# Kernel tuning notes

Measured on AMD Instinct MI355X. Metric: run time of the kernel, lower is better.

Reference implementation:

```python
import jax, jax.numpy as jnp
import numpy as np

T, B, D, H = 512, 64, 512, 512  # seq_len, batch, input_size, hidden_size


def setup_inputs() -> dict:
    key = jax.random.key(0)
    ks = jax.random.split(key, 7)
    s = jnp.float32(0.05)  # keep gates out of saturation
    return {
        "x": jax.random.normal(ks[0], (T, B, D), jnp.float32),
        "Wi_l0": jax.random.normal(ks[1], (2, 4 * H, D), jnp.float32) * s,
        "Wh_l0": jax.random.normal(ks[2], (2, 4 * H, H), jnp.float32) * s,
        "b_l0": jax.random.normal(ks[3], (2, 4 * H), jnp.float32) * s,
        "Wi_l1": jax.random.normal(ks[4], (2, 4 * H, 2 * H), jnp.float32) * s,
        "Wh_l1": jax.random.normal(ks[5], (2, 4 * H, H), jnp.float32) * s,
        "b_l1": jax.random.normal(ks[6], (2, 4 * H), jnp.float32) * s,
    }


def _lstm_dir(xs, Wi, Wh, b):
    """Run one LSTM direction over xs: [T, B, Din] -> ([T, B, H], h_T, c_T)."""
    Bsz = xs.shape[1]
    Hh = Wh.shape[-1]
    # Precompute input contribution for all timesteps (the big GEMM).
    gx = jnp.einsum('tbd,gd->tbg', xs, Wi) + b  # [T, B, 4H]

    def step(carry, gx_t):
        h, c = carry
        gates = gx_t + h @ Wh.T  # [B, 4H]
        i, f, g, o = jnp.split(gates, 4, axis=-1)
        c = jax.nn.sigmoid(f) * c + jax.nn.sigmoid(i) * jnp.tanh(g)
        h = jax.nn.sigmoid(o) * jnp.tanh(c)
        return (h, c), h

    h0 = jnp.zeros((Bsz, Hh), xs.dtype)
    (hT, cT), hs = jax.lax.scan(step, (h0, h0), gx)
    return hs, hT, cT


def _bilstm_layer(xs, Wi, Wh, b):
    hf, hTf, cTf = _lstm_dir(xs, Wi[0], Wh[0], b[0])
    hb, hTb, cTb = _lstm_dir(xs[::-1], Wi[1], Wh[1], b[1])
    # torch.stack(dim=2).view(T, B, -1) == concat along feature axis
    out = jnp.concatenate([hf, hb[::-1]], axis=-1)  # [T, B, 2H]
    return out, (hTf, hTb), (cTf, cTb)


def reference(x, Wi_l0, Wh_l0, b_l0, Wi_l1, Wh_l1, b_l1):
    o0, h0s, c0s = _bilstm_layer(x, Wi_l0, Wh_l0, b_l0)
    o1, h1s, c1s = _bilstm_layer(o0, Wi_l1, Wh_l1, b_l1)
    # state order: (layer0 fwd, layer0 bwd, layer1 fwd, layer1 bwd)
    h_n = jnp.stack(h0s + h1s, axis=0)  # [4, B, H]
    c_n = jnp.stack(c0s + c1s, axis=0)  # [4, B, H]
    return o1, (h_n, c_n)
```

## Files before the change

kernel.cpp:

```cpp
#include <hip/hip_runtime.h>
#include <stdint.h>


#define TT 512
#define BATCH 64
#define HH 512
#define NWG 64
#define NCOLS 32

typedef __attribute__((ext_vector_type(8))) short vshort8;
typedef __attribute__((ext_vector_type(4))) float vfloat4;

__device__ __forceinline__ vfloat4 mfma16(vshort8 a, vshort8 b, vfloat4 c) {
    return __builtin_amdgcn_mfma_f32_16x16x32_bf16(a, b, c, 0, 0, 0);
}

__device__ __forceinline__ float sigmoidf_(float x) {
    return 1.f / (1.f + __expf(-x));
}
__device__ __forceinline__ float tanhf_(float x) {
    float e = __expf(2.f * x);
    return 1.f - 2.f / (e + 1.f);
}
__device__ __forceinline__ unsigned short f2bf(float f) {
    uint32_t u = __float_as_uint(f);
    uint32_t r = (u + 0x7fffu + ((u >> 16) & 1u)) >> 16;
    return (unsigned short)r;
}

__global__ void cvt_f32_bf16(const float* __restrict__ src,
                             unsigned short* __restrict__ dst, int n) {
    int i = (blockIdx.x * blockDim.x + threadIdx.x) * 4;
    if (i + 3 < n) {
        float4 v = *(const float4*)(src + i);
        uint2 p;
        p.x = (uint32_t)f2bf(v.x) | ((uint32_t)f2bf(v.y) << 16);
        p.y = (uint32_t)f2bf(v.z) | ((uint32_t)f2bf(v.w) << 16);
        *(uint2*)(dst + i) = p;
    }
}

template <int DIN, bool WRITE_BF16>
__launch_bounds__(256, 1)
__global__ void lstm_phase(const unsigned short* __restrict__ A,
                           const unsigned short* __restrict__ Wi,
                           const float* __restrict__ Whf,
                           const float* __restrict__ bias,
                           unsigned short* __restrict__ hbuf,
                           uint32_t* __restrict__ cnt,
                           unsigned short* __restrict__ obf,
                           float* __restrict__ of32,
                           float* __restrict__ hn,
                           float* __restrict__ cn)
{
    __shared__ unsigned short Wlds[NCOLS * 1024];
    __shared__ unsigned short Wpad[16 * 1024];

    const int tid = threadIdx.x;
    ((volatile unsigned short*)Wpad)[tid] = 0;

    const int dir = blockIdx.x >> 6;
    const int wg = blockIdx.x & 63;
    const int j0 = wg * 8;
    const int lane = tid & 63;
    const int wave = tid >> 6;

    for (int chunk = tid; chunk < NCOLS * DIN / 8; chunk += 256) {
        int n = chunk / (DIN / 8);
        int k8 = (chunk % (DIN / 8)) * 8;
        int grow = (n >> 3) * HH + j0 + (n & 7);
        vshort8 v = *(const vshort8*)(Wi + ((size_t)dir * 4 * HH + grow) * DIN + k8);
        int byte = n * DIN * 2 + ((k8 * 2) ^ ((n & 7) << 4));
        *(vshort8*)((char*)Wlds + byte) = v;
    }
    __syncthreads();

    const int arow = wave * 16 + (lane & 15);
    const int kOff = (lane >> 4) * 8;
    const int klane = (lane >> 4) * 16;
    const int n0 = lane & 15;
    const int swz = (n0 & 7) << 4;
    const int nb0 = n0 * DIN * 2;
    const int nb1 = (16 + n0) * DIN * 2;
    const int grow0 = (n0 >> 3) * HH + j0 + (n0 & 7);
    const int grow1 = ((n0 >> 3) + 2) * HH + j0 + (n0 & 7);
    const float bias0 = bias[dir * 4 * HH + grow0];
    const float bias1 = bias[dir * 4 * HH + grow1];
    const bool lo = (lane & 8) == 0;
    const int jcol = j0 + (lane & 7);
    const int hrowb = wave * 16 + ((lane >> 4) << 2);
    uint32_t* const cline = cnt + (dir * 4 + wave) * 32;

    const float* whf0 = Whf + ((size_t)dir * 4 * HH + grow0) * HH + kOff;
    const float* whf1 = Whf + ((size_t)dir * 4 * HH + grow1) * HH + kOff;
    vshort8 wh0r[16], wh1r[16];
#pragma unroll
    for (int kk = 0; kk < 16; ++kk) {
        float4 a0 = *(const float4*)(whf0 + kk * 32);
        float4 a1 = *(const float4*)(whf0 + kk * 32 + 4);
        float4 b0 = *(const float4*)(whf1 + kk * 32);
        float4 b1 = *(const float4*)(whf1 + kk * 32 + 4);
        vshort8 a, b;
        a[0] = (short)f2bf(a0.x); a[1] = (short)f2bf(a0.y);
        a[2] = (short)f2bf(a0.z); a[3] = (short)f2bf(a0.w);
        a[4] = (short)f2bf(a1.x); a[5] = (short)f2bf(a1.y);
        a[6] = (short)f2bf(a1.z); a[7] = (short)f2bf(a1.w);
        b[0] = (short)f2bf(b0.x); b[1] = (short)f2bf(b0.y);
        b[2] = (short)f2bf(b0.z); b[3] = (short)f2bf(b0.w);
        b[4] = (short)f2bf(b1.x); b[5] = (short)f2bf(b1.y);
        b[6] = (short)f2bf(b1.z); b[7] = (short)f2bf(b1.w);
        wh0r[kk] = a;
        wh1r[kk] = b;
        asm volatile("" : "+v"(wh0r[kk]), "+v"(wh1r[kk]));
    }

    float cstate[4] = {0.f, 0.f, 0.f, 0.f};

    for (int s = 0; s < TT; ++s) {
        const int t = dir ? (TT - 1 - s) : s;

        vfloat4 acc0, acc1;
        acc0[0] = acc0[1] = acc0[2] = acc0[3] = bias0;
        acc1[0] = acc1[1] = acc1[2] = acc1[3] = bias1;

        const unsigned short* ap = A + ((size_t)t * BATCH + arow) * DIN + kOff;
#pragma unroll 8
        for (int kk = 0; kk < DIN / 32; ++kk) {
            vshort8 a = *(const vshort8*)(ap + kk * 32);
            int kb = kk * 64 + klane;
            vshort8 b0 = *(const vshort8*)((const char*)Wlds + nb0 + (kb ^ swz));
            vshort8 b1 = *(const vshort8*)((const char*)Wlds + nb1 + (kb ^ swz));
            acc0 = mfma16(a, b0, acc0);
            acc1 = mfma16(a, b1, acc1);
        }

        if (s > 0) {
            const uint32_t target = 64u * (uint32_t)s;
            for (;;) {
                uint32_t v;
                asm volatile(
                    "global_load_dword %0, %1, off sc0 sc1\n\t"
                    "s_waitcnt vmcnt(0)"
                    : "=v"(v) : "v"(cline) : "memory");
                if (__builtin_amdgcn_readfirstlane(v) >= target) break;
                __builtin_amdgcn_s_sleep(1);
            }
            __builtin_amdgcn_sched_barrier(0);

            const unsigned short* hp =
                hbuf + (((dir << 1) | ((s - 1) & 1)) * BATCH + arow) * HH + kOff;
            vshort8 hd[16];
#pragma unroll
            for (int kk = 0; kk < 16; ++kk)
                asm volatile("global_load_dwordx4 %0, %1, off sc0 sc1"
                             : "=v"(hd[kk]) : "v"(hp + kk * 32));
            asm volatile("s_waitcnt vmcnt(0)" ::: "memory");
            __builtin_amdgcn_sched_barrier(0);
#pragma unroll
            for (int kk = 0; kk < 16; ++kk) {
                acc0 = mfma16(hd[kk], wh0r[kk], acc0);
                acc1 = mfma16(hd[kk], wh1r[kk], acc1);
            }
        }

        float hval[4];
#pragma unroll
        for (int r = 0; r < 4; ++r) {
            float own0 = acc0[r], own1 = acc1[r];
            float oth0 = __shfl_xor(own0, 8, 64);
            float oth1 = __shfl_xor(own1, 8, 64);
            float iv = lo ? own0 : oth0;
            float fv = lo ? oth0 : own0;
            float gv = lo ? own1 : oth1;
            float ov = lo ? oth1 : own1;
            float cnew = sigmoidf_(fv) * cstate[r] + sigmoidf_(iv) * tanhf_(gv);
            cstate[r] = cnew;
            hval[r] = sigmoidf_(ov) * tanhf_(cnew);
        }

        unsigned short* hw = hbuf + (size_t)(((dir << 1) | (s & 1)) * BATCH) * HH;
        const int rA = lo ? 0 : 2;
        unsigned short hb[2];
        hb[0] = f2bf(hval[rA]);
        hb[1] = f2bf(hval[rA + 1]);
#pragma unroll
        for (int q = 0; q < 2; ++q) {
            int row = hrowb + rA + q;
            unsigned short* wp = hw + row * HH + jcol;
            uint32_t v32 = hb[q];
            asm volatile("global_store_short %0, %1, off sc0 sc1"
                         :: "v"(wp), "v"(v32) : "memory");
        }
        asm volatile("s_waitcnt vmcnt(0)" ::: "memory");
        __builtin_amdgcn_sched_barrier(0);
        if (lane == 0) atomicAdd((unsigned int*)cline, 1u);

#pragma unroll
        for (int q = 0; q < 2; ++q) {
            int row = hrowb + rA + q;
            if constexpr (WRITE_BF16)
                obf[((size_t)t * BATCH + row) * (2 * HH) + dir * HH + jcol] = hb[q];
            else
                of32[((size_t)t * BATCH + row) * (2 * HH) + dir * HH + jcol] =
                    hval[q == 0 ? rA : rA + 1];
        }
        if (s == TT - 1) {
#pragma unroll
            for (int q = 0; q < 2; ++q) {
                int r = rA + q, row = hrowb + r;
                hn[(dir * BATCH + row) * HH + jcol] = hval[r];
                cn[(dir * BATCH + row) * HH + jcol] = cstate[r];
            }
        }
    }
}

extern "C" void kernel_launch(void* const* d_in, const int* in_sizes, int n_in,
                              void* d_out, int out_size, void* d_ws, size_t ws_size,
                              hipStream_t stream) {
    const float* x = (const float*)d_in[0];
    const float* Wi0 = (const float*)d_in[1];
    const float* Wh0 = (const float*)d_in[2];
    const float* b0 = (const float*)d_in[3];
    const float* Wi1 = (const float*)d_in[4];
    const float* Wh1 = (const float*)d_in[5];
    const float* b1 = (const float*)d_in[6];

    char* ws = (char*)d_ws;
    uint32_t* cntA = (uint32_t*)(ws);
    uint32_t* cntB = (uint32_t*)(ws + 2048);
    unsigned short* hbufA = (unsigned short*)(ws + 8192);
    unsigned short* hbufB = (unsigned short*)(ws + 270336);
    unsigned short* wi0b = (unsigned short*)(ws + 1048576);
    unsigned short* wi1b = (unsigned short*)(ws + 5242880);
    unsigned short* xb = (unsigned short*)(ws + 13631488);
    unsigned short* o0 = (unsigned short*)(ws + 47185920);

    float* out = (float*)d_out;
    const size_t O1SZ = (size_t)TT * BATCH * 2 * HH;
    float* hn_base = out + O1SZ;
    float* cn_base = out + O1SZ + 4 * BATCH * HH;

    hipMemsetAsync(ws, 0, 4096, stream);

    {
        int n;
        n = TT * BATCH * 512;
        cvt_f32_bf16<<<n / 1024, 256, 0, stream>>>(x, xb, n);
        n = 2 * 2048 * 512;
        cvt_f32_bf16<<<n / 1024, 256, 0, stream>>>(Wi0, wi0b, n);
        n = 2 * 2048 * 1024;
        cvt_f32_bf16<<<n / 1024, 256, 0, stream>>>(Wi1, wi1b, n);
    }

    lstm_phase<512, true><<<128, 256, 0, stream>>>(
        xb, wi0b, Wh0, b0, hbufA, cntA, o0, nullptr, hn_base, cn_base);

    lstm_phase<1024, false><<<128, 256, 0, stream>>>(
        o0, wi1b, Wh1, b1, hbufB, cntB, nullptr, out,
        hn_base + 2 * BATCH * HH, cn_base + 2 * BATCH * HH);
}
```

Before: 7.380 ms.

## Split workgroup into producer waves for input GEMM and consumer recurrence waves

Doubles the workgroup to 512 threads. Four producer waves compute the per-step input projection (x·Wi + bias) ahead of time into a 4-slot LDS ring, while four consumer waves run only the recurrent h·Wh part and the gate math. The two sides hand off through LDS flag counters. The recurrent weights move from registers into swizzled LDS, which frees VGPRs but adds LDS reads on the serial critical path, and the new spin-wait handshakes add latency.

```diff
diff --git a/kernel.cpp b/kernel.cpp
--- a/kernel.cpp
+++ b/kernel.cpp
@@ -41,7 +41,7 @@
 }
 
 template <int DIN, bool WRITE_BF16>
-__launch_bounds__(256, 1)
+__launch_bounds__(512, 1)
 __global__ void lstm_phase(const unsigned short* __restrict__ A,
                            const unsigned short* __restrict__ Wi,
                            const float* __restrict__ Whf,
@@ -53,19 +53,23 @@
                            float* __restrict__ hn,
                            float* __restrict__ cn)
 {
-    __shared__ unsigned short Wlds[NCOLS * 1024];
-    __shared__ unsigned short Wpad[16 * 1024];
+    __shared__ unsigned short Wlds[NCOLS * DIN];
+    __shared__ unsigned short Whlds[NCOLS * HH];
+    __shared__ __align__(16) float gxT[4][NCOLS][68];
+    __shared__ int gxflag[4];
+    __shared__ int cflag[4][4];
 
     const int tid = threadIdx.x;
-    ((volatile unsigned short*)Wpad)[tid] = 0;
-
     const int dir = blockIdx.x >> 6;
     const int wg = blockIdx.x & 63;
     const int j0 = wg * 8;
     const int lane = tid & 63;
     const int wave = tid >> 6;
 
-    for (int chunk = tid; chunk < NCOLS * DIN / 8; chunk += 256) {
+    if (tid < 4) gxflag[tid] = 0;
+    if (tid >= 4 && tid < 20) cflag[(tid - 4) >> 2][(tid - 4) & 3] = 0;
+
+    for (int chunk = tid; chunk < NCOLS * DIN / 8; chunk += 512) {
         int n = chunk / (DIN / 8);
         int k8 = (chunk % (DIN / 8)) * 8;
         int grow = (n >> 3) * HH + j0 + (n & 7);
@@ -73,66 +77,111 @@
         int byte = n * DIN * 2 + ((k8 * 2) ^ ((n & 7) << 4));
         *(vshort8*)((char*)Wlds + byte) = v;
     }
+    for (int chunk = tid; chunk < NCOLS * HH / 8; chunk += 512) {
+        int n = chunk / (HH / 8);
+        int k8 = (chunk % (HH / 8)) * 8;
+        int grow = (n >> 3) * HH + j0 + (n & 7);
+        const float* src = Whf + ((size_t)dir * 4 * HH + grow) * HH + k8;
+        float4 f0 = *(const float4*)(src);
+        float4 f1 = *(const float4*)(src + 4);
+        vshort8 v;
+        v[0] = (short)f2bf(f0.x); v[1] = (short)f2bf(f0.y);
+        v[2] = (short)f2bf(f0.z); v[3] = (short)f2bf(f0.w);
+        v[4] = (short)f2bf(f1.x); v[5] = (short)f2bf(f1.y);
+        v[6] = (short)f2bf(f1.z); v[7] = (short)f2bf(f1.w);
+        int byte = n * HH * 2 + ((k8 * 2) ^ ((n & 7) << 4));
+        *(vshort8*)((char*)Whlds + byte) = v;
+    }
     __syncthreads();
 
-    const int arow = wave * 16 + (lane & 15);
     const int kOff = (lane >> 4) * 8;
     const int klane = (lane >> 4) * 16;
     const int n0 = lane & 15;
     const int swz = (n0 & 7) << 4;
-    const int nb0 = n0 * DIN * 2;
-    const int nb1 = (16 + n0) * DIN * 2;
-    const int grow0 = (n0 >> 3) * HH + j0 + (n0 & 7);
-    const int grow1 = ((n0 >> 3) + 2) * HH + j0 + (n0 & 7);
-    const float bias0 = bias[dir * 4 * HH + grow0];
-    const float bias1 = bias[dir * 4 * HH + grow1];
+
+    if (wave >= 4) {
+        const int p = wave - 4;
+        const int nb0 = n0 * DIN * 2;
+        const int nb1 = (16 + n0) * DIN * 2;
+        const int grow0 = (n0 >> 3) * HH + j0 + (n0 & 7);
+        const int grow1 = ((n0 >> 3) + 2) * HH + j0 + (n0 & 7);
+        const float bias0 = bias[dir * 4 * HH + grow0];
+        const float bias1 = bias[dir * 4 * HH + grow1];
+        float* const g0 = &gxT[p][n0][(lane >> 4) * 4];
+        float* const g1 = &gxT[p][16 + n0][(lane >> 4) * 4];
+
+        for (int s = p; s < TT; s += 4) {
+            if (s >= 4) {
+                for (;;) {
+                    int ok = 1;
+#pragma unroll
+                    for (int c2 = 0; c2 < 4; ++c2)
+                        ok &= (__hip_atomic_load(&cflag[p][c2], __ATOMIC_RELAXED,
+                                                 __HIP_MEMORY_SCOPE_WORKGROUP) >= s - 3);
+                    if (ok) break;
+                    __builtin_amdgcn_s_sleep(1);
+                }
+            }
+            const int t = dir ? (TT - 1 - s) : s;
+            vfloat4 xa0, xa1, xa2, xa3, xb0, xb1, xb2, xb3;
+            xa0[0]=xa0[1]=xa0[2]=xa0[3]=bias0; xa1=xa0; xa2=xa0; xa3=xa0;
+            xb0[0]=xb0[1]=xb0[2]=xb0[3]=bias1; xb1=xb0; xb2=xb0; xb3=xb0;
+
+            const unsigned short* ap =
+                A + ((size_t)t * BATCH + (lane & 15)) * DIN + kOff;
+#pragma unroll 4
+            for (int kk = 0; kk < DIN / 32; ++kk) {
+                int kb = kk * 64 + klane;
+                vshort8 b0 = *(const vshort8*)((const char*)Wlds + nb0 + (kb ^ swz));
+                vshort8 b1 = *(const vshort8*)((const char*)Wlds + nb1 + (kb ^ swz));
+                vshort8 a0 = *(const vshort8*)(ap + kk * 32);
+                vshort8 a1 = *(const vshort8*)(ap + (size_t)16 * DIN + kk * 32);
+                vshort8 a2 = *(const vshort8*)(ap + (size_t)32 * DIN + kk * 32);
+                vshort8 a3 = *(const vshort8*)(ap + (size_t)48 * DIN + kk * 32);
+                xa0 = mfma16(a0, b0, xa0); xb0 = mfma16(a0, b1, xb0);
+                xa1 = mfma16(a1, b0, xa1); xb1 = mfma16(a1, b1, xb1);
+                xa2 = mfma16(a2, b0, xa2); xb2 = mfma16(a2, b1, xb2);
+                xa3 = mfma16(a3, b0, xa3); xb3 = mfma16(a3, b1, xb3);
+            }
+            *(vfloat4*)(g0)      = xa0; *(vfloat4*)(g1)      = xb0;
+            *(vfloat4*)(g0 + 16) = xa1; *(vfloat4*)(g1 + 16) = xb1;
+            *(vfloat4*)(g0 + 32) = xa2; *(vfloat4*)(g1 + 32) = xb2;
+            *(vfloat4*)(g0 + 48) = xa3; *(vfloat4*)(g1 + 48) = xb3;
+            asm volatile("s_waitcnt lgkmcnt(0)" ::: "memory");
+            __hip_atomic_store(&gxflag[p], s + 1, __ATOMIC_RELAXED,
+                               __HIP_MEMORY_SCOPE_WORKGROUP);
+        }
+        return;
+    }
+
+    const int c = wave;
+    const int arow = c * 16 + (lane & 15);
+    const int nb0h = n0 * HH * 2;
+    const int nb1h = (16 + n0) * HH * 2;
     const bool lo = (lane & 8) == 0;
     const int jcol = j0 + (lane & 7);
-    const int hrowb = wave * 16 + ((lane >> 4) << 2);
-    uint32_t* const cline = cnt + (dir * 4 + wave) * 32;
-
-    const float* whf0 = Whf + ((size_t)dir * 4 * HH + grow0) * HH + kOff;
-    const float* whf1 = Whf + ((size_t)dir * 4 * HH + grow1) * HH + kOff;
-    vshort8 wh0r[16], wh1r[16];
-#pragma unroll
-    for (int kk = 0; kk < 16; ++kk) {
-        float4 a0 = *(const float4*)(whf0 + kk * 32);
-        float4 a1 = *(const float4*)(whf0 + kk * 32 + 4);
-        float4 b0 = *(const float4*)(whf1 + kk * 32);
-        float4 b1 = *(const float4*)(whf1 + kk * 32 + 4);
-        vshort8 a, b;
-        a[0] = (short)f2bf(a0.x); a[1] = (short)f2bf(a0.y);
-        a[2] = (short)f2bf(a0.z); a[3] = (short)f2bf(a0.w);
-        a[4] = (short)f2bf(a1.x); a[5] = (short)f2bf(a1.y);
-        a[6] = (short)f2bf(a1.z); a[7] = (short)f2bf(a1.w);
-        b[0] = (short)f2bf(b0.x); b[1] = (short)f2bf(b0.y);
-        b[2] = (short)f2bf(b0.z); b[3] = (short)f2bf(b0.w);
-        b[4] = (short)f2bf(b1.x); b[5] = (short)f2bf(b1.y);
-        b[6] = (short)f2bf(b1.z); b[7] = (short)f2bf(b1.w);
-        wh0r[kk] = a;
-        wh1r[kk] = b;
-        asm volatile("" : "+v"(wh0r[kk]), "+v"(wh1r[kk]));
-    }
+    const int hrowb = c * 16 + ((lane >> 4) << 2);
+    uint32_t* const cline = cnt + (dir * 4 + c) * 32;
+    const float* const gr0 = &gxT[0][n0][c * 16 + (lane >> 4) * 4];
+    const float* const gr1 = &gxT[0][16 + n0][c * 16 + (lane >> 4) * 4];
+    const int slotStride = NCOLS * 68;
 
     float cstate[4] = {0.f, 0.f, 0.f, 0.f};
 
     for (int s = 0; s < TT; ++s) {
         const int t = dir ? (TT - 1 - s) : s;
-
-        vfloat4 acc0, acc1;
-        acc0[0] = acc0[1] = acc0[2] = acc0[3] = bias0;
-        acc1[0] = acc1[1] = acc1[2] = acc1[3] = bias1;
-
-        const unsigned short* ap = A + ((size_t)t * BATCH + arow) * DIN + kOff;
-#pragma unroll 8
-        for (int kk = 0; kk < DIN / 32; ++kk) {
-            vshort8 a = *(const vshort8*)(ap + kk * 32);
-            int kb = kk * 64 + klane;
-            vshort8 b0 = *(const vshort8*)((const char*)Wlds + nb0 + (kb ^ swz));
-            vshort8 b1 = *(const vshort8*)((const char*)Wlds + nb1 + (kb ^ swz));
-            acc0 = mfma16(a, b0, acc0);
-            acc1 = mfma16(a, b1, acc1);
-        }
+        const int slot = s & 3;
+
+        while (__hip_atomic_load(&gxflag[slot], __ATOMIC_RELAXED,
+                                 __HIP_MEMORY_SCOPE_WORKGROUP) < s + 1)
+            __builtin_amdgcn_s_sleep(1);
+        vfloat4 acc0 = *(const vfloat4*)(gr0 + slot * slotStride);
+        vfloat4 acc1 = *(const vfloat4*)(gr1 + slot * slotStride);
+        asm volatile("s_waitcnt lgkmcnt(0)" ::: "memory");
+        __builtin_amdgcn_sched_barrier(0);
+        if (lane == 0)
+            __hip_atomic_store(&cflag[slot][c], s + 1, __ATOMIC_RELAXED,
+                               __HIP_MEMORY_SCOPE_WORKGROUP);
 
         if (s > 0) {
             const uint32_t target = 64u * (uint32_t)s;
@@ -158,8 +207,11 @@
             __builtin_amdgcn_sched_barrier(0);
 #pragma unroll
             for (int kk = 0; kk < 16; ++kk) {
-                acc0 = mfma16(hd[kk], wh0r[kk], acc0);
-                acc1 = mfma16(hd[kk], wh1r[kk], acc1);
+                int kb = kk * 64 + klane;
+                vshort8 b0 = *(const vshort8*)((const char*)Whlds + nb0h + (kb ^ swz));
+                vshort8 b1 = *(const vshort8*)((const char*)Whlds + nb1h + (kb ^ swz));
+                acc0 = mfma16(hd[kk], b0, acc0);
+                acc1 = mfma16(hd[kk], b1, acc1);
             }
         }
 
@@ -202,7 +254,7 @@
                 obf[((size_t)t * BATCH + row) * (2 * HH) + dir * HH + jcol] = hb[q];
             else
                 of32[((size_t)t * BATCH + row) * (2 * HH) + dir * HH + jcol] =
-                    hval[q == 0 ? rA : rA + 1];
+                    hval[rA + q];
         }
         if (s == TT - 1) {
 #pragma unroll
@@ -253,10 +305,10 @@
         cvt_f32_bf16<<<n / 1024, 256, 0, stream>>>(Wi1, wi1b, n);
     }
 
-    lstm_phase<512, true><<<128, 256, 0, stream>>>(
+    lstm_phase<512, true><<<128, 512, 0, stream>>>(
         xb, wi0b, Wh0, b0, hbufA, cntA, o0, nullptr, hn_base, cn_base);
 
-    lstm_phase<1024, false><<<128, 256, 0, stream>>>(
+    lstm_phase<1024, false><<<128, 512, 0, stream>>>(
         o0, wi1b, Wh1, b1, hbufB, cntB, nullptr, out,
         hn_base + 2 * BATCH * HH, cn_base + 2 * BATCH * HH);
 }
```

Result: slower. 8.827 ms (+19.6%).
